# Kernel optimization log

Hardware: AMD Instinct MI355X
Metric: run time of the kernel (lower is better)

The kernel has to match this reference:

```python
import jax, jax.numpy as jnp
import numpy as np

N_NODES = 50000
N_EDGES = 600000
IN_CH = 128
OUT_CH = 64
HID = 2 * OUT_CH  # 128


def setup_inputs() -> dict:
    key = jax.random.key(0)
    k1, k2, k3, k4 = jax.random.split(key, 4)
    x = jax.random.normal(k1, (N_NODES, IN_CH), dtype=jnp.float32)
    edge_index = jax.random.randint(k2, (2, N_EDGES), 0, N_NODES, dtype=jnp.int64)
    # Glorot-style init scale for linear weights (PyG GCNConv default init)
    W1 = jax.random.normal(k3, (IN_CH, HID), dtype=jnp.float32) * (1.0 / np.sqrt(IN_CH))
    b1 = jnp.zeros((HID,), dtype=jnp.float32)
    W2 = jax.random.normal(k4, (HID, OUT_CH), dtype=jnp.float32) * (1.0 / np.sqrt(HID))
    b2 = jnp.zeros((OUT_CH,), dtype=jnp.float32)
    return {"x": x, "edge_index": edge_index, "W1": W1, "b1": b1, "W2": W2, "b2": b2}


def _gcn_norm(edge_index, n_nodes):
    # Add self loops, then symmetric normalization: norm_e = d^-1/2[src] * d^-1/2[dst]
    loop = jnp.arange(n_nodes, dtype=edge_index.dtype)
    src = jnp.concatenate([edge_index[0], loop])
    dst = jnp.concatenate([edge_index[1], loop])
    deg = jax.ops.segment_sum(jnp.ones_like(dst, dtype=jnp.float32), dst, num_segments=n_nodes)
    dinv = jnp.where(deg > 0, jax.lax.rsqrt(deg), 0.0)
    norm = dinv[src] * dinv[dst]  # [E + N]
    return src, dst, norm


def _gcn_conv(x, src, dst, norm, W, b, n_nodes):
    h = x @ W                      # [N, d_out]  dense transform first (PyG order)
    msg = h[src] * norm[:, None]   # gather + scale: [E+N, d_out]
    agg = jax.ops.segment_sum(msg, dst, num_segments=n_nodes)  # scatter-add
    return agg + b


def reference(x, edge_index, W1, b1, W2, b2):
    n = x.shape[0]
    src, dst, norm = _gcn_norm(edge_index, n)  # shared (cached=True in original)
    h = jax.nn.relu(_gcn_conv(x, src, dst, norm, W1, b1, n))
    return _gcn_conv(h, src, dst, norm, W2, b2, n)
```

## Files before the change

kernel.cpp:

```cpp
#include <hip/hip_runtime.h>


typedef __attribute__((ext_vector_type(8))) short short8;
typedef __attribute__((ext_vector_type(4))) float float4v;

constexpr int PB = 128;
constexpr int PERS = 2048;

static __device__ __forceinline__ ushort f2bf(float f) {
  union { float f; unsigned u; } c; c.f = f;
  unsigned u = c.u;
  return (ushort)((u + 0x7fffu + ((u >> 16) & 1u)) >> 16);
}
static __device__ __forceinline__ float bf2f(ushort h) {
  union { unsigned u; float f; } c; c.u = ((unsigned)h) << 16;
  return c.f;
}
static __device__ __forceinline__ float bfhi(unsigned packed) {
  union { unsigned u; float f; } c; c.u = packed & 0xffff0000u;
  return c.f;
}
static __device__ __forceinline__ float bflo(unsigned packed) {
  union { unsigned u; float f; } c; c.u = packed << 16;
  return c.f;
}

struct MegaParams {
  const float* x;
  const int* src;
  const int* dst;
  const float* W1;
  const float* b1;
  const float* W2;
  const float* b2;
  int N, E, NBK, EPB, GB, NAGG;
  int* cnt_mat;
  int* bases;
  unsigned* part;
  int* row_ptr;
  float* dinv;
  int* col;
  ushort* h;
  ushort* h1hi;
  ushort* h1lo;
  ushort* h2;
  ushort* w1hi;
  ushort* w1lo;
  ushort* w2hi;
  ushort* w2lo;
  float* out;
};

static __device__ __forceinline__ void wswz_tile(const float* __restrict__ W,
                                                 ushort* __restrict__ whi,
                                                 ushort* __restrict__ wlo,
                                                 int M, int tile, int lane) {
  int ntiles = M >> 4;
  int kt = tile / ntiles, nt = tile % ntiles;
  int colg = nt * 16 + (lane & 15);
  int krow = kt * 32 + (lane >> 4) * 8;
  size_t o = ((size_t)tile * 64 + lane) * 8;
#pragma unroll
  for (int j = 0; j < 8; j++) {
    float v = W[(size_t)(krow + j) * M + colg];
    ushort h = f2bf(v);
    whi[o + j] = h;
    wlo[o + j] = f2bf(v - bf2f(h));
  }
}

__global__ __launch_bounds__(256) void k_g1(MegaParams P) {
  __shared__ int hist[512];
  int bid = blockIdx.x, t = threadIdx.x;
  if (bid >= PB) {
    int tile = (bid - PB) * 4 + (t >> 6);
    int lane = t & 63;
    if (tile < 32) wswz_tile(P.W1, P.w1hi, P.w1lo, 128, tile, lane);
    else           wswz_tile(P.W2, P.w2hi, P.w2lo, 64, tile - 32, lane);
    return;
  }
  for (int k = t; k < P.NBK; k += 256) hist[k] = 0;
  __syncthreads();
  int start = bid * P.EPB;
  int stop = min(P.E, start + P.EPB);
  for (int e = start + t * 4; e < stop; e += 1024) {
    if (e + 4 <= stop) {
      int4 d = *(const int4*)(P.dst + e);
      atomicAdd(&hist[d.x >> 7], 1);
      atomicAdd(&hist[d.y >> 7], 1);
      atomicAdd(&hist[d.z >> 7], 1);
      atomicAdd(&hist[d.w >> 7], 1);
    } else {
      for (int j = e; j < stop; j++) atomicAdd(&hist[P.dst[j] >> 7], 1);
    }
  }
  __syncthreads();
  for (int k = t; k < P.NBK; k += 256) P.cnt_mat[k * PB + bid] = hist[k];
}

static __device__ void gemm1_block(int gb, const MegaParams& P) {
  constexpr int K = 128, M = 128, NT = M / 16;
  int t = threadIdx.x;
  int lane = t & 63;
  int wv = t >> 6;
  int quad = lane >> 4, lo16 = lane & 15;
  int rowbase = gb * 64 + wv * 16;
  int arow = rowbase + lo16;
  bool arow_ok = arow < P.N;
  float4v acc[NT];
#pragma unroll
  for (int nt = 0; nt < NT; nt++) acc[nt] = (float4v){0.f, 0.f, 0.f, 0.f};
  for (int kt = 0; kt < 4; kt++) {
    short8 ahi, alo;
    float av[8];
    if (arow_ok) {
      const float* ap = P.x + (size_t)arow * K + kt * 32 + quad * 8;
      float4 a0 = *(const float4*)ap;
      float4 a1 = *(const float4*)(ap + 4);
      av[0] = a0.x; av[1] = a0.y; av[2] = a0.z; av[3] = a0.w;
      av[4] = a1.x; av[5] = a1.y; av[6] = a1.z; av[7] = a1.w;
    } else {
#pragma unroll
      for (int j = 0; j < 8; j++) av[j] = 0.f;
    }
#pragma unroll
    for (int j = 0; j < 8; j++) {
      ushort hh = f2bf(av[j]);
      ahi[j] = (short)hh;
      alo[j] = (short)f2bf(av[j] - bf2f(hh));
    }
    const ushort* ph = P.w1hi + ((size_t)(kt * NT) * 64 + lane) * 8;
    const ushort* pl = P.w1lo + ((size_t)(kt * NT) * 64 + lane) * 8;
#pragma unroll
    for (int nt = 0; nt < NT; nt++) {
      short8 bhi = *(const short8*)(ph + nt * 512);
      short8 blo = *(const short8*)(pl + nt * 512);
      acc[nt] = __builtin_amdgcn_mfma_f32_16x16x32_bf16(ahi, bhi, acc[nt], 0, 0, 0);
      acc[nt] = __builtin_amdgcn_mfma_f32_16x16x32_bf16(alo, bhi, acc[nt], 0, 0, 0);
      acc[nt] = __builtin_amdgcn_mfma_f32_16x16x32_bf16(ahi, blo, acc[nt], 0, 0, 0);
    }
  }
#pragma unroll
  for (int nt = 0; nt < NT; nt++) {
#pragma unroll
    for (int r = 0; r < 4; r++) {
      int row = rowbase + quad * 4 + r;
      if (row < P.N) P.h[(size_t)row * M + nt * 16 + lo16] = f2bf(acc[nt][r]);
    }
  }
}

__global__ __launch_bounds__(256) void k_g2(MegaParams P) {
  __shared__ int buf[256];
  __shared__ int base[512];
  __shared__ int tot[512];
  __shared__ int cur[512];
  int bid = blockIdx.x, t = threadIdx.x;
  if (bid >= PB) {
    gemm1_block(bid - PB, P);
    return;
  }
  for (int k = t; k < P.NBK; k += 256) {
    const int* row = P.cnt_mat + (size_t)k * PB;
    int pre = 0, s = 0;
    for (int b = 0; b < PB; b++) {
      int c = row[b];
      s += c;
      if (b < bid) pre += c;
    }
    tot[k] = s;
    cur[k] = pre;
  }
  __syncthreads();
  {
    int carry = 0;
    for (int b0 = 0; b0 < 512; b0 += 256) {
      int idx = b0 + t;
      int v = (idx < P.NBK) ? tot[idx] : 0;
      buf[t] = v;
      __syncthreads();
      for (int off = 1; off < 256; off <<= 1) {
        int add = (t >= off) ? buf[t - off] : 0;
        __syncthreads();
        buf[t] += add;
        __syncthreads();
      }
      base[idx] = carry + buf[t] - v;
      carry += buf[255];
      __syncthreads();
    }
  }
  for (int k = t; k < P.NBK; k += 256) cur[k] += base[k];
  if (bid == 0)
    for (int k = t; k <= P.NBK; k += 256) P.bases[k] = base[k];
  __syncthreads();
  int start = bid * P.EPB, stop = min(P.E, start + P.EPB);
  for (int e = start + t * 4; e < stop; e += 1024) {
    if (e + 4 <= stop) {
      int4 s = *(const int4*)(P.src + e);
      int4 d = *(const int4*)(P.dst + e);
      int p;
      p = atomicAdd(&cur[d.x >> 7], 1); P.part[p] = (unsigned)s.x | ((unsigned)(d.x & 127) << 25);
      p = atomicAdd(&cur[d.y >> 7], 1); P.part[p] = (unsigned)s.y | ((unsigned)(d.y & 127) << 25);
      p = atomicAdd(&cur[d.z >> 7], 1); P.part[p] = (unsigned)s.z | ((unsigned)(d.z & 127) << 25);
      p = atomicAdd(&cur[d.w >> 7], 1); P.part[p] = (unsigned)s.w | ((unsigned)(d.w & 127) << 25);
    } else {
      for (int j = e; j < stop; j++) {
        int p2 = atomicAdd(&cur[P.dst[j] >> 7], 1);
        P.part[p2] = (unsigned)P.src[j] | ((unsigned)(P.dst[j] & 127) << 25);
      }
    }
  }
}

__global__ __launch_bounds__(256) void k_g3(MegaParams P) {
  __shared__ int buf[256];
  __shared__ int cnt[128];
  __shared__ int cur[128];
  int bid = blockIdx.x, t = threadIdx.x;
  int beg = P.bases[bid], end = P.bases[bid + 1];
  if (t < 128) cnt[t] = 0;
  __syncthreads();
  for (int e = beg + t; e < end; e += 256) atomicAdd(&cnt[P.part[e] >> 25], 1);
  __syncthreads();
  int v = (t < 128) ? cnt[t] : 0;
  buf[t] = v;
  __syncthreads();
#pragma unroll
  for (int off = 1; off < 256; off <<= 1) {
    int add = (t >= off) ? buf[t - off] : 0;
    __syncthreads();
    buf[t] += add;
    __syncthreads();
  }
  if (t < 128) {
    int excl = buf[t] - v;
    cur[t] = beg + excl;
    int node = bid * 128 + t;
    if (node < P.N) {
      P.row_ptr[node] = beg + excl;
      P.dinv[node] = rsqrtf((float)(v + 1));
    }
  }
  if (bid == 0 && t == 0) P.row_ptr[P.N] = P.E;
  __syncthreads();
  for (int e = beg + t; e < end; e += 256) {
    unsigned p = P.part[e];
    int pos = atomicAdd(&cur[p >> 25], 1);
    P.col[pos] = (int)(p & 0x01FFFFFFu);
  }
}

template <int C, bool RELU, bool SPLIT>
static __device__ void agg_block(int vb, const MegaParams& P,
                                 const ushort* __restrict__ Hb,
                                 const float* __restrict__ bias,
                                 float* __restrict__ out,
                                 ushort* __restrict__ outhi,
                                 ushort* __restrict__ outlo) {
  constexpr int VPL = C / 64;
  int lane = threadIdx.x & 63;
  int v = vb * 4 + (threadIdx.x >> 6);
  if (v >= P.N) return;
  float dv = P.dinv[v];
  float acc0 = 0.f, acc1 = 0.f;
  auto loadp = [&](int s) -> unsigned {
    if (VPL == 2) return *(const unsigned*)(Hb + (size_t)s * C + lane * 2);
    else          return (unsigned)Hb[(size_t)s * C + lane];
  };
  {
    unsigned u = loadp(v);
    if (VPL == 2) { acc0 = dv * bflo(u); acc1 = dv * bfhi(u); }
    else          { acc0 = dv * bf2f((ushort)u); }
  }
  int beg = P.row_ptr[v], end = P.row_ptr[v + 1];
  for (int base = beg; base < end; base += 64) {
    int m = end - base;
    if (m > 64) m = 64;
    int sl = 0;
    float wl = 0.f;
    if (lane < m) {
      sl = P.col[base + lane];
      wl = P.dinv[sl];
    }
    int j = 0;
    for (; j + 8 <= m; j += 8) {
      int s[8]; float wq[8]; unsigned u[8];
#pragma unroll
      for (int q = 0; q < 8; q++) { s[q] = __shfl(sl, j + q); wq[q] = __shfl(wl, j + q); }
#pragma unroll
      for (int q = 0; q < 8; q++) u[q] = loadp(s[q]);
#pragma unroll
      for (int q = 0; q < 8; q++) {
        if (VPL == 2) {
          acc0 = fmaf(wq[q], bflo(u[q]), acc0);
          acc1 = fmaf(wq[q], bfhi(u[q]), acc1);
        } else {
          acc0 = fmaf(wq[q], bf2f((ushort)u[q]), acc0);
        }
      }
    }
    for (; j + 4 <= m; j += 4) {
      int s[4]; float wq[4]; unsigned u[4];
#pragma unroll
      for (int q = 0; q < 4; q++) { s[q] = __shfl(sl, j + q); wq[q] = __shfl(wl, j + q); }
#pragma unroll
      for (int q = 0; q < 4; q++) u[q] = loadp(s[q]);
#pragma unroll
      for (int q = 0; q < 4; q++) {
        if (VPL == 2) {
          acc0 = fmaf(wq[q], bflo(u[q]), acc0);
          acc1 = fmaf(wq[q], bfhi(u[q]), acc1);
        } else {
          acc0 = fmaf(wq[q], bf2f((ushort)u[q]), acc0);
        }
      }
    }
    for (; j < m; j++) {
      int s = __shfl(sl, j);
      float wv = __shfl(wl, j);
      unsigned u = loadp(s);
      if (VPL == 2) {
        acc0 = fmaf(wv, bflo(u), acc0);
        acc1 = fmaf(wv, bfhi(u), acc1);
      } else {
        acc0 = fmaf(wv, bf2f((ushort)u), acc0);
      }
    }
  }
  float r0 = fmaf(dv, acc0, bias[lane * VPL + 0]);
  if (RELU) r0 = fmaxf(r0, 0.f);
  if (VPL == 2) {
    float r1 = fmaf(dv, acc1, bias[lane * VPL + 1]);
    if (RELU) r1 = fmaxf(r1, 0.f);
    if (SPLIT) {
      ushort h0 = f2bf(r0), h1 = f2bf(r1);
      ushort l0 = f2bf(r0 - bf2f(h0)), l1 = f2bf(r1 - bf2f(h1));
      ((unsigned*)outhi)[(size_t)v * (C / 2) + lane] = (unsigned)h0 | ((unsigned)h1 << 16);
      ((unsigned*)outlo)[(size_t)v * (C / 2) + lane] = (unsigned)l0 | ((unsigned)l1 << 16);
    } else {
      *(float2*)&out[(size_t)v * C + lane * 2] = make_float2(r0, r1);
    }
  } else {
    out[(size_t)v * C + lane] = r0;
  }
}

static __device__ void gemm2_block(int gb, const MegaParams& P) {
  constexpr int K = 128, M = 64, NT = M / 16;
  int t = threadIdx.x;
  int lane = t & 63;
  int wv = t >> 6;
  int quad = lane >> 4, lo16 = lane & 15;
  int rowbase = gb * 64 + wv * 16;
  int arow = rowbase + lo16;
  bool arow_ok = arow < P.N;
  float4v acc[NT];
#pragma unroll
  for (int nt = 0; nt < NT; nt++) acc[nt] = (float4v){0.f, 0.f, 0.f, 0.f};
  for (int kt = 0; kt < 4; kt++) {
    short8 ahi, alo;
    if (arow_ok) {
      size_t ao = (size_t)arow * K + kt * 32 + quad * 8;
      ahi = *(const short8*)(P.h1hi + ao);
      alo = *(const short8*)(P.h1lo + ao);
    } else {
      ahi = (short8)0; alo = (short8)0;
    }
    const ushort* ph = P.w2hi + ((size_t)(kt * NT) * 64 + lane) * 8;
    const ushort* pl = P.w2lo + ((size_t)(kt * NT) * 64 + lane) * 8;
#pragma unroll
    for (int nt = 0; nt < NT; nt++) {
      short8 bhi = *(const short8*)(ph + nt * 512);
      short8 blo = *(const short8*)(pl + nt * 512);
      acc[nt] = __builtin_amdgcn_mfma_f32_16x16x32_bf16(ahi, bhi, acc[nt], 0, 0, 0);
      acc[nt] = __builtin_amdgcn_mfma_f32_16x16x32_bf16(alo, bhi, acc[nt], 0, 0, 0);
      acc[nt] = __builtin_amdgcn_mfma_f32_16x16x32_bf16(ahi, blo, acc[nt], 0, 0, 0);
    }
  }
#pragma unroll
  for (int nt = 0; nt < NT; nt++) {
#pragma unroll
    for (int r = 0; r < 4; r++) {
      int row = rowbase + quad * 4 + r;
      if (row < P.N) P.h2[(size_t)row * M + nt * 16 + lo16] = f2bf(acc[nt][r]);
    }
  }
}

__global__ __launch_bounds__(256) void k_g4(MegaParams P) {
  for (int vb = blockIdx.x; vb < P.NAGG; vb += gridDim.x)
    agg_block<128, true, true>(vb, P, P.h, P.b1, nullptr, P.h1hi, P.h1lo);
}
__global__ __launch_bounds__(256) void k_g5(MegaParams P) {
  for (int gb = blockIdx.x; gb < P.GB; gb += gridDim.x) gemm2_block(gb, P);
}
__global__ __launch_bounds__(256) void k_g6(MegaParams P) {
  for (int vb = blockIdx.x; vb < P.NAGG; vb += gridDim.x)
    agg_block<64, false, false>(vb, P, P.h2, P.b2, P.out, nullptr, nullptr);
}

extern "C" void kernel_launch(void* const* d_in, const int* in_sizes, int n_in,
                              void* d_out, int out_size, void* d_ws, size_t ws_size,
                              hipStream_t stream) {
  MegaParams P;
  P.x  = (const float*)d_in[0];
  const int* ei = (const int*)d_in[1];
  P.W1 = (const float*)d_in[2];
  P.b1 = (const float*)d_in[3];
  P.W2 = (const float*)d_in[4];
  P.b2 = (const float*)d_in[5];
  P.N = in_sizes[0] / 128;
  P.E = in_sizes[1] / 2;
  P.src = ei;
  P.dst = ei + P.E;
  P.NBK = (P.N + 127) / 128;
  P.EPB = ((P.E + PB - 1) / PB + 3) & ~3;
  P.GB = (P.N + 63) / 64;
  P.NAGG = (P.N + 3) / 4;

  auto al = [](size_t v) { return (v + 255) & ~(size_t)255; };
  char* w = (char*)d_ws;
  P.cnt_mat = (int*)w;      w += al((size_t)P.NBK * PB * 4);
  P.bases   = (int*)w;      w += al((size_t)(P.NBK + 1) * 4);
  P.part    = (unsigned*)w; w += al((size_t)P.E * 4);
  P.row_ptr = (int*)w;      w += al((size_t)(P.N + 1) * 4);
  P.dinv    = (float*)w;    w += al((size_t)P.N * 4);
  P.col     = (int*)w;      w += al((size_t)P.E * 4);
  P.h       = (ushort*)w;   w += al((size_t)P.N * 128 * 2);
  P.h1hi    = (ushort*)w;   w += al((size_t)P.N * 128 * 2);
  P.h1lo    = (ushort*)w;   w += al((size_t)P.N * 128 * 2);
  P.h2      = (ushort*)w;   w += al((size_t)P.N * 64 * 2);
  P.w1hi    = (ushort*)w;   w += al((size_t)128 * 128 * 2);
  P.w1lo    = (ushort*)w;   w += al((size_t)128 * 128 * 2);
  P.w2hi    = (ushort*)w;   w += al((size_t)128 * 64 * 2);
  P.w2lo    = (ushort*)w;   w += al((size_t)128 * 64 * 2);
  P.out = (float*)d_out;

  k_g1<<<PB + 12, 256, 0, stream>>>(P);
  k_g2<<<PB + P.GB, 256, 0, stream>>>(P);
  k_g3<<<P.NBK, 256, 0, stream>>>(P);
  k_g4<<<PERS, 256, 0, stream>>>(P);
  k_g5<<<1024, 256, 0, stream>>>(P);
  k_g6<<<PERS, 256, 0, stream>>>(P);
}
```

Baseline: 170.8 us.

## Fuse layer-1 aggregation with second GEMM via shared-memory tile

The layer-1 neighbour aggregation now writes its fp32 rows into a shared-memory tile of 64 nodes per block. The same block then splits them into bf16 hi/lo and runs the MFMA GEMM with W2 directly. This removes the global h1hi/h1lo intermediate buffers and one kernel launch, avoiding a write and re-read of about 25MB. In exchange, each wave processes 16 nodes serially with a non-persistent grid, and the block must finish its whole aggregation before the GEMM, which may reduce latency hiding and load balance.

```diff
diff --git a/kernel.cpp b/kernel.cpp
--- a/kernel.cpp
+++ b/kernel.cpp
@@ -6,6 +6,7 @@
 
 constexpr int PB = 128;
 constexpr int PERS = 2048;
+constexpr int LDW = 132;
 
 static __device__ __forceinline__ ushort f2bf(float f) {
   union { float f; unsigned u; } c; c.f = f;
@@ -41,8 +42,6 @@
   float* dinv;
   int* col;
   ushort* h;
-  ushort* h1hi;
-  ushort* h1lo;
   ushort* h2;
   ushort* w1hi;
   ushort* w1lo;
@@ -251,28 +250,129 @@
   }
 }
 
-template <int C, bool RELU, bool SPLIT>
-static __device__ void agg_block(int vb, const MegaParams& P,
-                                 const ushort* __restrict__ Hb,
-                                 const float* __restrict__ bias,
-                                 float* __restrict__ out,
-                                 ushort* __restrict__ outhi,
-                                 ushort* __restrict__ outlo) {
-  constexpr int VPL = C / 64;
+__global__ __launch_bounds__(256) void k_g4(MegaParams P) {
+  __shared__ float h1t[64 * LDW];
+  int b = blockIdx.x;
+  int t = threadIdx.x;
+  int lane = t & 63, wv = t >> 6;
+  int v0 = b * 64 + wv * 16;
+  int rp = 0;
+  float dvl = 0.f;
+  if (lane < 17) {
+    int vv = v0 + lane;
+    rp = (vv <= P.N) ? P.row_ptr[vv] : P.E;
+  }
+  if (lane < 16) {
+    int vv = v0 + lane;
+    dvl = (vv < P.N) ? P.dinv[vv] : 0.f;
+  }
+#pragma unroll 1
+  for (int i = 0; i < 16; i++) {
+    int rl = wv * 16 + i;
+    int v = v0 + i;
+    float acc0 = 0.f, acc1 = 0.f;
+    if (v < P.N) {
+      float dv = __shfl(dvl, i);
+      int beg = __shfl(rp, i), end = __shfl(rp, i + 1);
+      unsigned su = *(const unsigned*)(P.h + (size_t)v * 128 + lane * 2);
+      acc0 = dv * bflo(su);
+      acc1 = dv * bfhi(su);
+      for (int base = beg; base < end; base += 64) {
+        int m = end - base;
+        if (m > 64) m = 64;
+        int sl = 0;
+        float wl = 0.f;
+        if (lane < m) {
+          sl = P.col[base + lane];
+          wl = P.dinv[sl];
+        }
+        int j = 0;
+        for (; j + 8 <= m; j += 8) {
+          int s[8]; float wq[8]; unsigned u[8];
+#pragma unroll
+          for (int q = 0; q < 8; q++) { s[q] = __shfl(sl, j + q); wq[q] = __shfl(wl, j + q); }
+#pragma unroll
+          for (int q = 0; q < 8; q++) u[q] = *(const unsigned*)(P.h + (size_t)s[q] * 128 + lane * 2);
+#pragma unroll
+          for (int q = 0; q < 8; q++) {
+            acc0 = fmaf(wq[q], bflo(u[q]), acc0);
+            acc1 = fmaf(wq[q], bfhi(u[q]), acc1);
+          }
+        }
+        for (; j + 4 <= m; j += 4) {
+          int s[4]; float wq[4]; unsigned u[4];
+#pragma unroll
+          for (int q = 0; q < 4; q++) { s[q] = __shfl(sl, j + q); wq[q] = __shfl(wl, j + q); }
+#pragma unroll
+          for (int q = 0; q < 4; q++) u[q] = *(const unsigned*)(P.h + (size_t)s[q] * 128 + lane * 2);
+#pragma unroll
+          for (int q = 0; q < 4; q++) {
+            acc0 = fmaf(wq[q], bflo(u[q]), acc0);
+            acc1 = fmaf(wq[q], bfhi(u[q]), acc1);
+          }
+        }
+        for (; j < m; j++) {
+          int s = __shfl(sl, j);
+          float ww = __shfl(wl, j);
+          unsigned u = *(const unsigned*)(P.h + (size_t)s * 128 + lane * 2);
+          acc0 = fmaf(ww, bflo(u), acc0);
+          acc1 = fmaf(ww, bfhi(u), acc1);
+        }
+      }
+      acc0 = fmaf(dv, acc0, P.b1[lane * 2 + 0]);
+      acc1 = fmaf(dv, acc1, P.b1[lane * 2 + 1]);
+      acc0 = fmaxf(acc0, 0.f);
+      acc1 = fmaxf(acc1, 0.f);
+    }
+    *(float2*)&h1t[rl * LDW + lane * 2] = make_float2(acc0, acc1);
+  }
+  __syncthreads();
+  constexpr int NT = 4;
+  int quad = lane >> 4, lo16 = lane & 15;
+  float4v acc[NT];
+#pragma unroll
+  for (int nt = 0; nt < NT; nt++) acc[nt] = (float4v){0.f, 0.f, 0.f, 0.f};
+  for (int kt = 0; kt < 4; kt++) {
+    const float* ap = &h1t[(wv * 16 + lo16) * LDW + kt * 32 + quad * 8];
+    float4 a0 = *(const float4*)ap;
+    float4 a1 = *(const float4*)(ap + 4);
+    float av[8];
+    av[0] = a0.x; av[1] = a0.y; av[2] = a0.z; av[3] = a0.w;
+    av[4] = a1.x; av[5] = a1.y; av[6] = a1.z; av[7] = a1.w;
+    short8 ahi, alo;
+#pragma unroll
+    for (int j = 0; j < 8; j++) {
+      ushort hh = f2bf(av[j]);
+      ahi[j] = (short)hh;
+      alo[j] = (short)f2bf(av[j] - bf2f(hh));
+    }
+    const ushort* ph = P.w2hi + ((size_t)(kt * NT) * 64 + lane) * 8;
+    const ushort* pl = P.w2lo + ((size_t)(kt * NT) * 64 + lane) * 8;
+#pragma unroll
+    for (int nt = 0; nt < NT; nt++) {
+      short8 bhi = *(const short8*)(ph + nt * 512);
+      short8 blo = *(const short8*)(pl + nt * 512);
+      acc[nt] = __builtin_amdgcn_mfma_f32_16x16x32_bf16(ahi, bhi, acc[nt], 0, 0, 0);
+      acc[nt] = __builtin_amdgcn_mfma_f32_16x16x32_bf16(alo, bhi, acc[nt], 0, 0, 0);
+      acc[nt] = __builtin_amdgcn_mfma_f32_16x16x32_bf16(ahi, blo, acc[nt], 0, 0, 0);
+    }
+  }
+#pragma unroll
+  for (int nt = 0; nt < NT; nt++) {
+#pragma unroll
+    for (int r = 0; r < 4; r++) {
+      int row = b * 64 + wv * 16 + quad * 4 + r;
+      if (row < P.N) P.h2[(size_t)row * 64 + nt * 16 + lo16] = f2bf(acc[nt][r]);
+    }
+  }
+}
+
+static __device__ void agg2_block(int vb, const MegaParams& P) {
   int lane = threadIdx.x & 63;
   int v = vb * 4 + (threadIdx.x >> 6);
   if (v >= P.N) return;
   float dv = P.dinv[v];
-  float acc0 = 0.f, acc1 = 0.f;
-  auto loadp = [&](int s) -> unsigned {
-    if (VPL == 2) return *(const unsigned*)(Hb + (size_t)s * C + lane * 2);
-    else          return (unsigned)Hb[(size_t)s * C + lane];
-  };
-  {
-    unsigned u = loadp(v);
-    if (VPL == 2) { acc0 = dv * bflo(u); acc1 = dv * bfhi(u); }
-    else          { acc0 = dv * bf2f((ushort)u); }
-  }
+  float acc0 = dv * bf2f(P.h2[(size_t)v * 64 + lane]);
   int beg = P.row_ptr[v], end = P.row_ptr[v + 1];
   for (int base = beg; base < end; base += 64) {
     int m = end - base;
@@ -285,119 +385,35 @@
     }
     int j = 0;
     for (; j + 8 <= m; j += 8) {
-      int s[8]; float wq[8]; unsigned u[8];
+      int s[8]; float wq[8]; ushort u[8];
 #pragma unroll
       for (int q = 0; q < 8; q++) { s[q] = __shfl(sl, j + q); wq[q] = __shfl(wl, j + q); }
 #pragma unroll
-      for (int q = 0; q < 8; q++) u[q] = loadp(s[q]);
-#pragma unroll
-      for (int q = 0; q < 8; q++) {
-        if (VPL == 2) {
-          acc0 = fmaf(wq[q], bflo(u[q]), acc0);
-          acc1 = fmaf(wq[q], bfhi(u[q]), acc1);
-        } else {
-          acc0 = fmaf(wq[q], bf2f((ushort)u[q]), acc0);
-        }
-      }
+      for (int q = 0; q < 8; q++) u[q] = P.h2[(size_t)s[q] * 64 + lane];
+#pragma unroll
+      for (int q = 0; q < 8; q++) acc0 = fmaf(wq[q], bf2f(u[q]), acc0);
     }
     for (; j + 4 <= m; j += 4) {
-      int s[4]; float wq[4]; unsigned u[4];
+      int s[4]; float wq[4]; ushort u[4];
 #pragma unroll
       for (int q = 0; q < 4; q++) { s[q] = __shfl(sl, j + q); wq[q] = __shfl(wl, j + q); }
 #pragma unroll
-      for (int q = 0; q < 4; q++) u[q] = loadp(s[q]);
-#pragma unroll
-      for (int q = 0; q < 4; q++) {
-        if (VPL == 2) {
-          acc0 = fmaf(wq[q], bflo(u[q]), acc0);
-          acc1 = fmaf(wq[q], bfhi(u[q]), acc1);
-        } else {
-          acc0 = fmaf(wq[q], bf2f((ushort)u[q]), acc0);
-        }
-      }
+      for (int q = 0; q < 4; q++) u[q] = P.h2[(size_t)s[q] * 64 + lane];
+#pragma unroll
+      for (int q = 0; q < 4; q++) acc0 = fmaf(wq[q], bf2f(u[q]), acc0);
     }
     for (; j < m; j++) {
       int s = __shfl(sl, j);
-      float wv = __shfl(wl, j);
-      unsigned u = loadp(s);
-      if (VPL == 2) {
-        acc0 = fmaf(wv, bflo(u), acc0);
-        acc1 = fmaf(wv, bfhi(u), acc1);
-      } else {
-        acc0 = fmaf(wv, bf2f((ushort)u), acc0);
-      }
-    }
-  }
-  float r0 = fmaf(dv, acc0, bias[lane * VPL + 0]);
-  if (RELU) r0 = fmaxf(r0, 0.f);
-  if (VPL == 2) {
-    float r1 = fmaf(dv, acc1, bias[lane * VPL + 1]);
-    if (RELU) r1 = fmaxf(r1, 0.f);
-    if (SPLIT) {
-      ushort h0 = f2bf(r0), h1 = f2bf(r1);
-      ushort l0 = f2bf(r0 - bf2f(h0)), l1 = f2bf(r1 - bf2f(h1));
-      ((unsigned*)outhi)[(size_t)v * (C / 2) + lane] = (unsigned)h0 | ((unsigned)h1 << 16);
-      ((unsigned*)outlo)[(size_t)v * (C / 2) + lane] = (unsigned)l0 | ((unsigned)l1 << 16);
-    } else {
-      *(float2*)&out[(size_t)v * C + lane * 2] = make_float2(r0, r1);
-    }
-  } else {
-    out[(size_t)v * C + lane] = r0;
-  }
-}
-
-static __device__ void gemm2_block(int gb, const MegaParams& P) {
-  constexpr int K = 128, M = 64, NT = M / 16;
-  int t = threadIdx.x;
-  int lane = t & 63;
-  int wv = t >> 6;
-  int quad = lane >> 4, lo16 = lane & 15;
-  int rowbase = gb * 64 + wv * 16;
-  int arow = rowbase + lo16;
-  bool arow_ok = arow < P.N;
-  float4v acc[NT];
-#pragma unroll
-  for (int nt = 0; nt < NT; nt++) acc[nt] = (float4v){0.f, 0.f, 0.f, 0.f};
-  for (int kt = 0; kt < 4; kt++) {
-    short8 ahi, alo;
-    if (arow_ok) {
-      size_t ao = (size_t)arow * K + kt * 32 + quad * 8;
-      ahi = *(const short8*)(P.h1hi + ao);
-      alo = *(const short8*)(P.h1lo + ao);
-    } else {
-      ahi = (short8)0; alo = (short8)0;
-    }
-    const ushort* ph = P.w2hi + ((size_t)(kt * NT) * 64 + lane) * 8;
-    const ushort* pl = P.w2lo + ((size_t)(kt * NT) * 64 + lane) * 8;
-#pragma unroll
-    for (int nt = 0; nt < NT; nt++) {
-      short8 bhi = *(const short8*)(ph + nt * 512);
-      short8 blo = *(const short8*)(pl + nt * 512);
-      acc[nt] = __builtin_amdgcn_mfma_f32_16x16x32_bf16(ahi, bhi, acc[nt], 0, 0, 0);
-      acc[nt] = __builtin_amdgcn_mfma_f32_16x16x32_bf16(alo, bhi, acc[nt], 0, 0, 0);
-      acc[nt] = __builtin_amdgcn_mfma_f32_16x16x32_bf16(ahi, blo, acc[nt], 0, 0, 0);
-    }
-  }
-#pragma unroll
-  for (int nt = 0; nt < NT; nt++) {
-#pragma unroll
-    for (int r = 0; r < 4; r++) {
-      int row = rowbase + quad * 4 + r;
-      if (row < P.N) P.h2[(size_t)row * M + nt * 16 + lo16] = f2bf(acc[nt][r]);
-    }
-  }
-}
-
-__global__ __launch_bounds__(256) void k_g4(MegaParams P) {
-  for (int vb = blockIdx.x; vb < P.NAGG; vb += gridDim.x)
-    agg_block<128, true, true>(vb, P, P.h, P.b1, nullptr, P.h1hi, P.h1lo);
-}
+      float ww = __shfl(wl, j);
+      acc0 = fmaf(ww, bf2f(P.h2[(size_t)s * 64 + lane]), acc0);
+    }
+  }
+  float r0 = fmaf(dv, acc0, P.b2[lane]);
+  P.out[(size_t)v * 64 + lane] = r0;
+}
+
 __global__ __launch_bounds__(256) void k_g5(MegaParams P) {
-  for (int gb = blockIdx.x; gb < P.GB; gb += gridDim.x) gemm2_block(gb, P);
-}
-__global__ __launch_bounds__(256) void k_g6(MegaParams P) {
-  for (int vb = blockIdx.x; vb < P.NAGG; vb += gridDim.x)
-    agg_block<64, false, false>(vb, P, P.h2, P.b2, P.out, nullptr, nullptr);
+  for (int vb = blockIdx.x; vb < P.NAGG; vb += gridDim.x) agg2_block(vb, P);
 }
 
 extern "C" void kernel_launch(void* const* d_in, const int* in_sizes, int n_in,
@@ -428,8 +444,6 @@
   P.dinv    = (float*)w;    w += al((size_t)P.N * 4);
   P.col     = (int*)w;      w += al((size_t)P.E * 4);
   P.h       = (ushort*)w;   w += al((size_t)P.N * 128 * 2);
-  P.h1hi    = (ushort*)w;   w += al((size_t)P.N * 128 * 2);
-  P.h1lo    = (ushort*)w;   w += al((size_t)P.N * 128 * 2);
   P.h2      = (ushort*)w;   w += al((size_t)P.N * 64 * 2);
   P.w1hi    = (ushort*)w;   w += al((size_t)128 * 128 * 2);
   P.w1lo    = (ushort*)w;   w += al((size_t)128 * 128 * 2);
@@ -440,7 +454,6 @@
   k_g1<<<PB + 12, 256, 0, stream>>>(P);
   k_g2<<<PB + P.GB, 256, 0, stream>>>(P);
   k_g3<<<P.NBK, 256, 0, stream>>>(P);
-  k_g4<<<PERS, 256, 0, stream>>>(P);
-  k_g5<<<1024, 256, 0, stream>>>(P);
-  k_g6<<<PERS, 256, 0, stream>>>(P);
-}
+  k_g4<<<P.GB, 256, 0, stream>>>(P);
+  k_g5<<<PERS, 256, 0, stream>>>(P);
+}
```

Measured after the change: 179.4 us. +5.0%, slower.
